# Optimization experiments

Measured on AMD Instinct MI355X. Metric: run time of the kernel, lower is better.

Reference implementation:

```python
import jax, jax.numpy as jnp
import numpy as np

B, C, G = 8, 64, 65536
IN_DIM, OUT_DIM = 64, 64
SLOPE = 0.1


def setup_inputs() -> dict:
    key = jax.random.key(0)
    ks = jax.random.split(key, 5)
    features = jax.random.normal(ks[0], (B, C, G), dtype=jnp.float32)
    # Conv2d(in*2, out, 1, bias=False) weights, squeezed to [out, in*2]
    W0 = jax.random.normal(ks[1], (OUT_DIM, IN_DIM * 2), dtype=jnp.float32) * (1.0 / np.sqrt(IN_DIM * 2))
    W1 = jax.random.normal(ks[2], (OUT_DIM, OUT_DIM * 2), dtype=jnp.float32) * (1.0 / np.sqrt(OUT_DIM * 2))
    W2 = jax.random.normal(ks[3], (OUT_DIM, OUT_DIM * 2), dtype=jnp.float32) * (1.0 / np.sqrt(OUT_DIM * 2))
    W3 = jax.random.normal(ks[4], (OUT_DIM, OUT_DIM * 2), dtype=jnp.float32) * (1.0 / np.sqrt(OUT_DIM * 2))
    return {"features": features, "W0": W0, "W1": W1, "W2": W2, "W3": W3}


def _layer(x, W):
    # x: [B, C, G]; tile the first group's features and build (x, x - x0)
    x0 = x[:, :, :1]                               # [B, C, 1]
    h = jnp.concatenate([x, x - x0], axis=1)       # [B, 2C, G]
    # 1x1 conv == pointwise linear over channels
    y = jnp.einsum("oc,bcg->bog", W, h)            # [B, O, G]
    return jax.nn.leaky_relu(y, negative_slope=SLOPE)


def reference(features, W0, W1, W2, W3):
    x = features
    for W in (W0, W1, W2, W3):
        x = _layer(x, W)
    return jnp.max(x, axis=-1)                     # [B, O]
```

## Files before the change

kernel.cpp:

```cpp
#include <hip/hip_runtime.h>


#define G_TOT 65536

typedef _Float16 hf2 __attribute__((ext_vector_type(2)));
typedef _Float16 hf4 __attribute__((ext_vector_type(4)));
typedef _Float16 hf8 __attribute__((ext_vector_type(8)));
typedef float float4_ __attribute__((ext_vector_type(4)));

static __device__ __forceinline__ hf2 pkh(float x, float y) {
    return __builtin_bit_cast(hf2, __builtin_amdgcn_cvt_pkrtz(x, y));
}


__global__ __launch_bounds__(256) void ge_prep(
    const float* __restrict__ feat,
    const float* __restrict__ W0, const float* __restrict__ W1,
    const float* __restrict__ W2, const float* __restrict__ W3,
    float* __restrict__ ws)
{
    const int tid = threadIdx.x;
    const int blk = blockIdx.x;
    __shared__ float lw[64][129];
    __shared__ float x0[2][64];

    if (blk == 8) {
        unsigned* maxenc = (unsigned*)(ws + 18432);
        maxenc[tid] = 0u; maxenc[tid + 256] = 0u;
        _Float16* wf = (_Float16*)ws;
        for (int ci = tid; ci < 8192; ci += 256) {
            int f = ci >> 8, ln = (ci >> 2) & 63, h2 = ci & 3;
            int l = f >> 3, mt = (f >> 1) & 3, pr = f & 1;
            int o = (mt << 4) + (ln & 15);
            int c = (pr << 5) + ((h2 >> 1) << 4) + ((ln >> 4) << 2) + ((h2 & 1) << 1);
            const float* Wl = (l == 0) ? W0 : (l == 1) ? W1 : (l == 2) ? W2 : W3;
            float a0 = Wl[o * 128 + c]     + Wl[o * 128 + 64 + c];
            float a1 = Wl[o * 128 + c + 1] + Wl[o * 128 + 64 + c + 1];
            *(hf2*)&wf[ci << 1] = pkh(a0, a1);
        }
        return;
    }

    const int b = blk;
    if (tid < 64) x0[0][tid] = feat[(size_t)(b * 64 + tid) * G_TOT];
    float* nbias = ws + 16384;
    for (int l = 0; l < 4; ++l) {
        const float* Wl = (l == 0) ? W0 : (l == 1) ? W1 : (l == 2) ? W2 : W3;
        for (int i = tid; i < 64 * 128; i += 256) lw[i >> 7][i & 127] = Wl[i];
        __syncthreads();
        if (tid < 64) {
            const int o = tid;
            const float* src = x0[l & 1];
            float s1 = 0.f, s2 = 0.f;
            for (int c = 0; c < 64; ++c) {
                float xv = src[c];
                s1 += lw[o][c] * xv;
                s2 += lw[o][64 + c] * xv;
            }
            nbias[b * 256 + l * 64 + o] = -s2;
            x0[(l & 1) ^ 1][o] = fmaxf(s1, 0.1f * s1);
        }
        __syncthreads();
    }
}

#define COMPUTE_TILE(BF)                                                              \
    _Pragma("unroll")                                                                 \
    for (int l = 0; l < 4; ++l) {                                                     \
        float4_ acc[4];                                                               \
        _Pragma("unroll")                                                             \
        for (int mt = 0; mt < 4; ++mt) {                                              \
            if (l < 3) acc[mt] = *(const float4_*)&lbias[(l << 6) + (mt << 4) + (q << 2)]; \
            else       acc[mt] = float4_{0.f, 0.f, 0.f, 0.f};                         \
        }                                                                             \
        _Pragma("unroll")                                                             \
        for (int mt = 0; mt < 4; ++mt) {                                              \
            _Pragma("unroll")                                                         \
            for (int pr = 0; pr < 2; ++pr) {                                          \
                union { hf8 h8; hf4 h4[2]; } ua;                                      \
                ua.h8 = *(const hf8*)&lwf[((((((l << 2) + mt) << 1) + pr) << 6) + lane) << 3]; \
                acc[mt] = __builtin_amdgcn_mfma_f32_16x16x16f16(ua.h4[0], BF[(pr << 1) + 0], acc[mt], 0, 0, 0); \
                acc[mt] = __builtin_amdgcn_mfma_f32_16x16x16f16(ua.h4[1], BF[(pr << 1) + 1], acc[mt], 0, 0, 0); \
            }                                                                         \
        }                                                                             \
        if (l < 3) {                                                                  \
            _Pragma("unroll")                                                         \
            for (int mt = 0; mt < 4; ++mt) {                                          \
                union { hf2 h2[2]; hf4 h4; } u;                                       \
                u.h2[0] = pkh(acc[mt][0], acc[mt][1]);                                \
                u.h2[1] = pkh(acc[mt][2], acc[mt][3]);                                \
                hf4 h = u.h4;                                                         \
                h = __builtin_elementwise_max(h, h * k01);                            \
                BF[mt] = h;                                                           \
            }                                                                         \
        } else {                                                                      \
            _Pragma("unroll")                                                         \
            for (int mt = 0; mt < 4; ++mt)                                            \
                _Pragma("unroll")                                                     \
                for (int j = 0; j < 4; ++j)                                           \
                    rmax[mt][j] = fmaxf(rmax[mt][j], acc[mt][j]);                     \
        }                                                                             \
    }

#define STAGE(PCOL, BUFBASE)                                                          \
    _Pragma("unroll")                                                                 \
    for (int j = 0; j < 4; ++j) {                                                     \
        const int G_ = (w << 2) + j;                                                  \
        const float* src_ = Fbase + (size_t)((G_ << 2) + (lane >> 4)) * G_TOT         \
                          + (PCOL) + ((lane & 15) << 2);                              \
        __builtin_amdgcn_global_load_lds(                                             \
            (const __attribute__((address_space(1))) unsigned*)src_,                  \
            (__attribute__((address_space(3))) unsigned*)&stg[(BUFBASE) + G_ * 272],  \
            16, 0, 0);                                                                \
    }

__global__ __launch_bounds__(256, 2) void ge_main(
    const float* __restrict__ feat,
    const float* __restrict__ ws_wf,
    const float* __restrict__ nbias,
    unsigned* __restrict__ maxenc)
{
    __shared__ __align__(16) float stg[2 * 16 * 272];
    __shared__ __align__(16) _Float16 lwf[16384];
    __shared__ float lbias[256];
    __shared__ float blockmax[4][64];
    const int tid = threadIdx.x;

    const int nb = ((blockIdx.x & 7) << 6) | (blockIdx.x >> 3);
    const int b = nb >> 6;
    const int w = tid >> 6, lane = tid & 63, q = lane >> 4, n = lane & 15;

    const float* Fbase = feat + (size_t)b * 64 * G_TOT + (size_t)((nb & 63) << 10);

    STAGE(0, 0)
    {
        const float4_* wp = (const float4_*)ws_wf;
#pragma unroll
        for (int i = 0; i < 8; ++i)
            *(float4_*)&lwf[(tid + (i << 8)) << 3] = wp[tid + (i << 8)];
    }
    lbias[tid] = nbias[(b << 8) + tid];

    float rmax[4][4];
#pragma unroll
    for (int mt = 0; mt < 4; ++mt)
#pragma unroll
        for (int j = 0; j < 4; ++j) rmax[mt][j] = -__builtin_inff();

    const hf4 k01 = { (_Float16)0.1f, (_Float16)0.1f, (_Float16)0.1f, (_Float16)0.1f };

    int curbase = 0;
#pragma unroll 1
    for (int p = 0; p < 16; ++p) {
        __syncthreads();
        if (p < 15) { STAGE((p + 1) << 6, curbase ^ 4352) }
        hf4 bf[4];
#pragma unroll
        for (int kf = 0; kf < 4; ++kf) {
            const int gb = curbase + ((kf << 2) + q) * 272 + (w << 4) + n;
            float f0 = stg[gb];
            float f1 = stg[gb + 64];
            float f2 = stg[gb + 128];
            float f3 = stg[gb + 192];
            union { hf2 h2[2]; hf4 h4; } u;
            u.h2[0] = pkh(f0, f1); u.h2[1] = pkh(f2, f3);
            bf[kf] = u.h4;
        }
        COMPUTE_TILE(bf)
        curbase ^= 4352;
    }

#pragma unroll
    for (int mt = 0; mt < 4; ++mt)
#pragma unroll
        for (int j = 0; j < 4; ++j) {
            float v = rmax[mt][j];
            v = fmaxf(v, __shfl_xor(v, 1, 64));
            v = fmaxf(v, __shfl_xor(v, 2, 64));
            v = fmaxf(v, __shfl_xor(v, 4, 64));
            v = fmaxf(v, __shfl_xor(v, 8, 64));
            rmax[mt][j] = v;
        }
    if (n == 0) {
#pragma unroll
        for (int mt = 0; mt < 4; ++mt)
#pragma unroll
            for (int j = 0; j < 4; ++j)
                blockmax[w][(mt << 4) + (q << 2) + j] = rmax[mt][j];
    }
    __syncthreads();
    if (tid < 64) {
        float v = fmaxf(fmaxf(blockmax[0][tid], blockmax[1][tid]),
                        fmaxf(blockmax[2][tid], blockmax[3][tid]));
        unsigned s = __float_as_uint(v);
        unsigned enc = (s & 0x80000000u) ? ~s : (s | 0x80000000u);
        atomicMax(&maxenc[b * 64 + tid], enc);
    }
}

__global__ void ge_final(const unsigned* __restrict__ maxenc,
                         const float* __restrict__ nbias,
                         float* __restrict__ out)
{
    int i = threadIdx.x;
    if (i < 512) {
        unsigned u = maxenc[i];
        unsigned s = (u & 0x80000000u) ? (u ^ 0x80000000u) : ~u;
        float v = __uint_as_float(s) + nbias[((i >> 6) << 8) + 192 + (i & 63)];
        out[i] = fmaxf(v, 0.1f * v);
    }
}

extern "C" void kernel_launch(void* const* d_in, const int* in_sizes, int n_in,
                              void* d_out, int out_size, void* d_ws, size_t ws_size,
                              hipStream_t stream) {
    const float* feat = (const float*)d_in[0];
    const float* W0 = (const float*)d_in[1];
    const float* W1 = (const float*)d_in[2];
    const float* W2 = (const float*)d_in[3];
    const float* W3 = (const float*)d_in[4];
    float* ws = (float*)d_ws;
    unsigned* maxenc = (unsigned*)(ws + 18432);

    ge_prep<<<9, 256, 0, stream>>>(feat, W0, W1, W2, W3, ws);
    ge_main<<<512, 256, 0, stream>>>(feat, ws, ws + 16384, maxenc);
    ge_final<<<1, 512, 0, stream>>>(maxenc, ws + 16384, (float*)d_out);
}
```

Baseline: 219.9 us.

## Triple-buffer feature staging, keep layer-0 weights in registers, add setprio

Expands the LDS staging ring from two to three buffers so loads run two tiles ahead, and replaces __syncthreads with explicit vmcnt waits plus an s_barrier. To fit LDS, the first layer's weight fragments now live in registers and only layers 1-3 stay in shared memory. s_setprio raises wave priority around the MFMA section. Register pressure rises with launch_bounds(256,2), which may cause spills or lower occupancy.

Result: no change. 222.9 us (+1.4%).

```diff
diff --git a/kernel.cpp b/kernel.cpp
--- a/kernel.cpp
+++ b/kernel.cpp
@@ -78,7 +78,8 @@
             _Pragma("unroll")                                                         \
             for (int pr = 0; pr < 2; ++pr) {                                          \
                 union { hf8 h8; hf4 h4[2]; } ua;                                      \
-                ua.h8 = *(const hf8*)&lwf[((((((l << 2) + mt) << 1) + pr) << 6) + lane) << 3]; \
+                if (l == 0) ua.h8 = wfr0[mt][pr];                                     \
+                else ua.h8 = *(const hf8*)&lwf[(((((((l - 1) << 2) + mt) << 1) + pr) << 6) + lane) * 8]; \
                 acc[mt] = __builtin_amdgcn_mfma_f32_16x16x16f16(ua.h4[0], BF[(pr << 1) + 0], acc[mt], 0, 0, 0); \
                 acc[mt] = __builtin_amdgcn_mfma_f32_16x16x16f16(ua.h4[1], BF[(pr << 1) + 1], acc[mt], 0, 0, 0); \
             }                                                                         \
@@ -120,8 +121,8 @@
     const float* __restrict__ nbias,
     unsigned* __restrict__ maxenc)
 {
-    __shared__ __align__(16) float stg[2 * 16 * 272];
-    __shared__ __align__(16) _Float16 lwf[16384];
+    __shared__ __align__(16) float stg[3 * 16 * 272];
+    __shared__ __align__(16) _Float16 lwf[12288];
     __shared__ float lbias[256];
     __shared__ float blockmax[4][64];
     const int tid = threadIdx.x;
@@ -132,14 +133,27 @@
 
     const float* Fbase = feat + (size_t)b * 64 * G_TOT + (size_t)((nb & 63) << 10);
 
+    hf8 wfr0[4][2];
+    {
+        const hf8* wp = (const hf8*)ws_wf;
+#pragma unroll
+        for (int mt = 0; mt < 4; ++mt)
+#pragma unroll
+            for (int pr = 0; pr < 2; ++pr)
+                wfr0[mt][pr] = wp[(((mt << 1) + pr) << 6) + lane];
+    }
+    {
+        const float4_* wp4 = (const float4_*)ws_wf;
+#pragma unroll
+        for (int k = 0; k < 6; ++k) {
+            int i = tid + (k << 8);
+            *(float4_*)&lwf[i << 3] = wp4[512 + i];
+        }
+    }
+    lbias[tid] = nbias[(b << 8) + tid];
+
     STAGE(0, 0)
-    {
-        const float4_* wp = (const float4_*)ws_wf;
-#pragma unroll
-        for (int i = 0; i < 8; ++i)
-            *(float4_*)&lwf[(tid + (i << 8)) << 3] = wp[tid + (i << 8)];
-    }
-    lbias[tid] = nbias[(b << 8) + tid];
+    STAGE(64, 4352)
 
     float rmax[4][4];
 #pragma unroll
@@ -149,15 +163,19 @@
 
     const hf4 k01 = { (_Float16)0.1f, (_Float16)0.1f, (_Float16)0.1f, (_Float16)0.1f };
 
-    int curbase = 0;
+    int rb = 0, sb = 8704;
 #pragma unroll 1
     for (int p = 0; p < 16; ++p) {
-        __syncthreads();
-        if (p < 15) { STAGE((p + 1) << 6, curbase ^ 4352) }
+        if (p < 15) asm volatile("s_waitcnt vmcnt(4) lgkmcnt(0)" ::: "memory");
+        else        asm volatile("s_waitcnt vmcnt(0) lgkmcnt(0)" ::: "memory");
+        __builtin_amdgcn_sched_barrier(0);
+        __builtin_amdgcn_s_barrier();
+        __builtin_amdgcn_sched_barrier(0);
+        if (p < 14) { STAGE((p + 2) << 6, sb) }
         hf4 bf[4];
 #pragma unroll
         for (int kf = 0; kf < 4; ++kf) {
-            const int gb = curbase + ((kf << 2) + q) * 272 + (w << 4) + n;
+            const int gb = rb + ((kf << 2) + q) * 272 + (w << 4) + n;
             float f0 = stg[gb];
             float f1 = stg[gb + 64];
             float f2 = stg[gb + 128];
@@ -166,8 +184,11 @@
             u.h2[0] = pkh(f0, f1); u.h2[1] = pkh(f2, f3);
             bf[kf] = u.h4;
         }
+        __builtin_amdgcn_s_setprio(1);
         COMPUTE_TILE(bf)
-        curbase ^= 4352;
+        __builtin_amdgcn_s_setprio(0);
+        rb = (rb == 8704) ? 0 : rb + 4352;
+        sb = (sb == 8704) ? 0 : sb + 4352;
     }
 
 #pragma unroll
```
